# Kernel tuning notes

Measured on AMD Instinct MI355X. Metric: run time of the kernel, lower is better.

The kernel has to match this reference:

```python
import jax, jax.numpy as jnp
import numpy as np
from jax import lax

STRIDE = (1, 1)
PADDING = ((1, 1), (1, 1))
DILATION = (1, 1)


def setup_inputs() -> dict:
    key = jax.random.key(0)
    k1, k2 = jax.random.split(key)
    input = jax.random.normal(k1, (32, 128, 56, 56), dtype=jnp.float32)
    weight = jax.random.normal(k2, (256, 128, 3, 3), dtype=jnp.float32)
    bias = jnp.zeros((256,), dtype=jnp.float32)
    return {"input": input, "weight": weight, "bias": bias}


def reference(input, weight, bias):
    # The original builds the conv's dense matrix via conv2d on an identity
    # basis and then matmuls; that is mathematically identical to a direct
    # conv2d (the map is linear), plus the broadcast bias.
    out = lax.conv_general_dilated(
        input, weight,
        window_strides=STRIDE,
        padding=PADDING,
        rhs_dilation=DILATION,
        dimension_numbers=("NCHW", "OIHW", "NCHW"),
    )
    return out + bias[None, :, None, None]
```

## Files before the change

kernel.cpp:

```cpp
#include <hip/hip_runtime.h>
#include <hip/hip_bf16.h>
#include <stdint.h>


typedef __attribute__((ext_vector_type(8))) short bf16x8;
typedef __attribute__((ext_vector_type(8))) unsigned short ushort8;
typedef __attribute__((ext_vector_type(4))) float f32x4;

#define HW       56
#define SPATIAL  3136
#define C_IN     128
#define K_OUT    256
#define GEMM_K   1152
#define GEMM_N   100352

#define PHW      58
#define PIMG     3364
#define PADTOT_AL 107656

#define BM       256
#define BN       256
#define NTILE    18
#define BUFH     32768

__device__ __forceinline__ unsigned short f2bf(float f) {
    union { float f; unsigned int u; } v; v.f = f;
    unsigned int u = v.u + 0x7FFFu + ((v.u >> 16) & 1u);
    return (unsigned short)(u >> 16);
}

__device__ __forceinline__ void gload16(const unsigned short* g, unsigned short* l) {
    __builtin_amdgcn_global_load_lds(
        (const __attribute__((address_space(1))) unsigned int*)(g),
        (__attribute__((address_space(3))) unsigned int*)(l),
        16, 0, 0);
}

__global__ __launch_bounds__(256)
void prep_kernel(const float* __restrict__ w, unsigned short* __restrict__ w3,
                 unsigned short* __restrict__ pad) {
    if (blockIdx.x < 1152) {
        int idx = blockIdx.x * 256 + threadIdx.x;
        int rc   = idx / 18432;
        int rem  = idx % 18432;
        int tap  = rem / 2048;
        int rem2 = rem % 2048;
        int cc   = rem2 / 512;
        int s    = rem2 % 512;
        int l    = s >> 3, j = s & 7;
        int ko   = rc * 16 + (l & 15);
        int c    = cc * 32 + ((l >> 4) << 3) + j;
        w3[idx] = f2bf(w[(ko * C_IN + c) * 9 + tap]);
    } else {
        int idx = (blockIdx.x - 1152) * 256 + threadIdx.x;
        if (idx >= 29184) return;
        int cc  = idx / 7296;
        int r   = idx % 7296;
        int img = r / 228;
        int p   = r % 228;
        int pos;
        if (p < 58)       pos = p;
        else if (p < 116) pos = 57 * PHW + (p - 58);
        else { int i = p - 116; pos = (1 + (i >> 1)) * PHW + (i & 1) * 57; }
        unsigned short* d = pad + (size_t)cc * PADTOT_AL * 32
                          + ((size_t)img * PIMG + pos) * 32;
        const ushort8 z = (ushort8){0,0,0,0,0,0,0,0};
        *reinterpret_cast<ushort8*>(d)      = z;
        *reinterpret_cast<ushort8*>(d + 8)  = z;
        *reinterpret_cast<ushort8*>(d + 16) = z;
        *reinterpret_cast<ushort8*>(d + 24) = z;
    }
}

__global__ __launch_bounds__(256)
void intrans_kernel(const float* __restrict__ in, unsigned short* __restrict__ pad) {
    __shared__ __attribute__((aligned(16))) unsigned short l[56 * 136];
    const int bx = blockIdx.x;
    const int n = bx / HW, h = bx % HW;
    const int tid = threadIdx.x;
    const float* src = in + (size_t)n * C_IN * SPATIAL + h * HW;
    #pragma unroll
    for (int i = 0; i < 28; ++i) {
        int idx = i * 256 + tid;
        int c = idx / HW, w = idx % HW;
        l[w * 136 + c] = f2bf(src[(size_t)c * SPATIAL + w]);
    }
    __syncthreads();
    const int prow = n * PIMG + (h + 1) * PHW;
    #pragma unroll
    for (int j = 0; j < 4; ++j) {
        int chunk = j * 256 + tid;
        if (chunk < 896) {
            int w = chunk >> 4, c8 = chunk & 15;
            int cc = c8 >> 2, sub = c8 & 3;
            unsigned short* dst = pad + (size_t)cc * PADTOT_AL * 32
                                + (size_t)(prow + w + 1) * 32 + sub * 8;
            *reinterpret_cast<ushort8*>(dst) =
                *reinterpret_cast<const ushort8*>(&l[w * 136 + c8 * 8]);
        }
    }
}

__global__ __launch_bounds__(1024, 1)
void conv_tlp2(const unsigned short* __restrict__ pad,
               const unsigned short* __restrict__ w3,
               const float* __restrict__ bias,
               float* __restrict__ out) {
    __shared__ __attribute__((aligned(16))) unsigned short lds[2 * BUFH];

    const int tid  = threadIdx.x;
    const int wave = tid >> 6;
    const int lane = tid & 63;
    const int la   = lane & 15;
    const int lkh  = lane >> 4;

    const int bid = blockIdx.x;
    const int nt  = (bid & 7) * 49 + (bid >> 3);
    const int g0  = nt * BN;

    const int wr = wave >> 2, wc = wave & 3;

    const unsigned short* aw = w3 + (size_t)wave * 18432 + lane * 8;
    const unsigned short* bsrc;
    {
        int col = g0 + wave * 16 + la;
        int img = col / SPATIAL;
        int pos = col - img * SPATIAL;
        int oh  = pos / HW, ow = pos - oh * HW;
        bsrc = pad + (size_t)(img * PIMG + (oh + 1) * PHW + (ow + 1)) * 32 + lkh * 8;
    }

    f32x4 acc[4][4];
    #pragma unroll
    for (int i = 0; i < 4; ++i)
        #pragma unroll
        for (int j = 0; j < 4; ++j)
            acc[i][j] = (f32x4){0.f, 0.f, 0.f, 0.f};

    auto STAGE = [&](int tn, int kc) {
        const int tap = tn >> 1;
        const int cc  = (tn & 1) * 2 + kc;
        const int dr = tap / 3 - 1, dsx = tap % 3 - 1;
        unsigned short* dst = &lds[(tn & 1) * BUFH];
        gload16(aw + (size_t)(tap * 4 + cc) * 512, dst + (wave * 2 + kc) * 512);
        gload16(bsrc + (size_t)cc * (PADTOT_AL * 32) + (dr * PHW + dsx) * 32,
                dst + 16384 + (wave * 2 + kc) * 512);
    };

    bf16x8 af0[4], af1[4], bv0[4], bv1[4];

    STAGE(0, 0); STAGE(0, 1); STAGE(1, 0);
    asm volatile("s_waitcnt vmcnt(2)" ::: "memory");
    __builtin_amdgcn_s_barrier();

    #pragma unroll
    for (int t = 0; t < NTILE; ++t) {
        const unsigned short* Ab = &lds[(t & 1) * BUFH];

        #pragma unroll
        for (int mi = 0; mi < 4; ++mi)
            af0[mi] = *reinterpret_cast<const bf16x8*>(
                &Ab[((wr * 4 + mi) * 2 + 0) * 512 + lane * 8]);
        #pragma unroll
        for (int nj = 0; nj < 4; ++nj)
            bv0[nj] = *reinterpret_cast<const bf16x8*>(
                &Ab[16384 + ((wc * 4 + nj) * 2 + 0) * 512 + lane * 8]);
        #pragma unroll
        for (int mi = 0; mi < 4; ++mi)
            af1[mi] = *reinterpret_cast<const bf16x8*>(
                &Ab[((wr * 4 + mi) * 2 + 1) * 512 + lane * 8]);

        asm volatile("s_waitcnt lgkmcnt(4)" ::: "memory");
        __builtin_amdgcn_sched_barrier(0);
        __builtin_amdgcn_s_setprio(1);
        #pragma unroll
        for (int mi = 0; mi < 4; ++mi)
            #pragma unroll
            for (int nj = 0; nj < 4; ++nj)
                acc[mi][nj] = __builtin_amdgcn_mfma_f32_16x16x32_bf16(
                    af0[mi], bv0[nj], acc[mi][nj], 0, 0, 0);
        __builtin_amdgcn_s_setprio(0);

        __builtin_amdgcn_s_barrier();

        #pragma unroll
        for (int nj = 0; nj < 4; ++nj)
            bv1[nj] = *reinterpret_cast<const bf16x8*>(
                &Ab[16384 + ((wc * 4 + nj) * 2 + 1) * 512 + lane * 8]);
        if (t + 1 < NTILE) STAGE(t + 1, 1);
        if (t + 2 < NTILE) STAGE(t + 2, 0);

        asm volatile("s_waitcnt lgkmcnt(0)" ::: "memory");
        __builtin_amdgcn_sched_barrier(0);
        __builtin_amdgcn_s_setprio(1);
        #pragma unroll
        for (int mi = 0; mi < 4; ++mi)
            #pragma unroll
            for (int nj = 0; nj < 4; ++nj)
                acc[mi][nj] = __builtin_amdgcn_mfma_f32_16x16x32_bf16(
                    af1[mi], bv1[nj], acc[mi][nj], 0, 0, 0);
        __builtin_amdgcn_s_setprio(0);

        if (t < NTILE - 2) {
            asm volatile("s_waitcnt vmcnt(2)" ::: "memory");
            __builtin_amdgcn_s_barrier();
        } else if (t == NTILE - 2) {
            asm volatile("s_waitcnt vmcnt(0)" ::: "memory");
            __builtin_amdgcn_s_barrier();
        }
    }

    #pragma unroll
    for (int mi = 0; mi < 4; ++mi) {
        const int mb = wr * 64 + mi * 16 + lkh * 4;
        const f32x4 bv4 = *reinterpret_cast<const f32x4*>(&bias[mb]);
        #pragma unroll
        for (int nj = 0; nj < 4; ++nj) {
            const int gcol = g0 + wc * 64 + nj * 16;
            const int n2 = gcol / SPATIAL;
            const int p2 = gcol - n2 * SPATIAL + la;
            float* op = out + ((size_t)(n2 * K_OUT + mb)) * SPATIAL + p2;
            op[0]                   = acc[mi][nj][0] + bv4[0];
            op[SPATIAL]             = acc[mi][nj][1] + bv4[1];
            op[2 * SPATIAL]         = acc[mi][nj][2] + bv4[2];
            op[3 * (size_t)SPATIAL] = acc[mi][nj][3] + bv4[3];
        }
    }
}

#define LDK 40
__global__ __launch_bounds__(256)
void conv_mfma_fallback(const float* __restrict__ in,
                        const float* __restrict__ wraw,
                        const float* __restrict__ bias,
                        float* __restrict__ out) {
    __shared__ __attribute__((aligned(16))) unsigned short lA[128 * LDK];
    __shared__ __attribute__((aligned(16))) unsigned short lB[128 * LDK];
    const int tid = threadIdx.x;
    const int m0  = blockIdx.y * 128;
    const int g0  = blockIdx.x * 128;
    const int wave = tid >> 6, lane = tid & 63;
    const int wr = wave >> 1, wc = wave & 1;
    const int la = lane & 15, lkh = lane >> 4, lk = lkh * 8;

    f32x4 acc[4][4];
    #pragma unroll
    for (int i = 0; i < 4; ++i)
        #pragma unroll
        for (int j = 0; j < 4; ++j)
            acc[i][j] = (f32x4){0.f, 0.f, 0.f, 0.f};

    const int jj = tid & 127;
    const int kb = (tid >> 7) * 16;
    const int g = g0 + jj;
    const int nimg = g / SPATIAL;
    const int pos  = g % SPATIAL;
    const int oh = pos / HW, ow = pos % HW;

    for (int tap = 0; tap < 9; ++tap) {
        const int dr = tap / 3 - 1, dsx = tap % 3 - 1;
        const int ih = oh + dr, iw = ow + dsx;
        const bool valid = ((unsigned)ih < HW) && ((unsigned)iw < HW);
        const float* src = in + ((nimg * C_IN) * HW + ih) * HW + iw;
        for (int c0 = 0; c0 < C_IN; c0 += 32) {
            #pragma unroll
            for (int i = 0; i < 2; ++i) {
                const int ch = tid * 2 + i;
                const int row = ch >> 2;
                const int kp = (ch & 3) * 8;
                ushort8 v;
                #pragma unroll
                for (int e = 0; e < 8; ++e)
                    v[e] = f2bf(wraw[((m0 + row) * C_IN + c0 + kp + e) * 9 + tap]);
                *reinterpret_cast<ushort8*>(&lA[row * LDK + kp]) = v;
            }
            {
                ushort8 v0, v1;
                #pragma unroll
                for (int i = 0; i < 8; ++i)
                    v0[i] = f2bf(valid ? src[(c0 + kb + i) * SPATIAL] : 0.f);
                #pragma unroll
                for (int i = 0; i < 8; ++i)
                    v1[i] = f2bf(valid ? src[(c0 + kb + 8 + i) * SPATIAL] : 0.f);
                *reinterpret_cast<ushort8*>(&lB[jj * LDK + kb])     = v0;
                *reinterpret_cast<ushort8*>(&lB[jj * LDK + kb + 8]) = v1;
            }
            __syncthreads();
            bf16x8 af[4], bv[4];
            #pragma unroll
            for (int f = 0; f < 4; ++f) {
                af[f] = *reinterpret_cast<const bf16x8*>(&lA[(wr * 64 + f * 16 + la) * LDK + lk]);
                bv[f] = *reinterpret_cast<const bf16x8*>(&lB[(wc * 64 + f * 16 + la) * LDK + lk]);
            }
            #pragma unroll
            for (int fi = 0; fi < 4; ++fi)
                #pragma unroll
                for (int fj = 0; fj < 4; ++fj)
                    acc[fi][fj] = __builtin_amdgcn_mfma_f32_16x16x32_bf16(
                        af[fi], bv[fj], acc[fi][fj], 0, 0, 0);
            __syncthreads();
        }
    }
    const int mbase = m0 + wr * 64;
    const int cbase = g0 + wc * 64;
    #pragma unroll
    for (int fi = 0; fi < 4; ++fi) {
        float bvv[4];
        #pragma unroll
        for (int r = 0; r < 4; ++r)
            bvv[r] = bias[mbase + fi * 16 + lkh * 4 + r];
        #pragma unroll
        for (int fj = 0; fj < 4; ++fj) {
            const int gcol = cbase + fj * 16 + la;
            const int n2 = gcol / SPATIAL;
            const int p2 = gcol % SPATIAL;
            float* op = out + (size_t)(n2 * K_OUT) * SPATIAL + p2;
            #pragma unroll
            for (int r = 0; r < 4; ++r)
                op[(size_t)(mbase + fi * 16 + lkh * 4 + r) * SPATIAL] = acc[fi][fj][r] + bvv[r];
        }
    }
}

extern "C" void kernel_launch(void* const* d_in, const int* in_sizes, int n_in,
                              void* d_out, int out_size, void* d_ws, size_t ws_size,
                              hipStream_t stream) {
    const float* in   = (const float*)d_in[0];
    const float* w    = (const float*)d_in[1];
    const float* bias = (const float*)d_in[2];
    float* out = (float*)d_out;

    const size_t pad_halves = 4ull * PADTOT_AL * 32ull;
    const size_t need_bytes = (pad_halves + 294912ull) * 2ull;

    if (ws_size >= need_bytes) {
        unsigned short* pad = (unsigned short*)d_ws;
        unsigned short* w3  = pad + pad_halves;
        prep_kernel<<<1152 + 114, 256, 0, stream>>>(w, w3, pad);
        intrans_kernel<<<32 * HW, 256, 0, stream>>>(in, pad);
        conv_tlp2<<<GEMM_N / BN, 1024, 0, stream>>>(pad, w3, bias, out);
    } else {
        dim3 grid(GEMM_N / 128, K_OUT / 128);
        conv_mfma_fallback<<<grid, 256, 0, stream>>>(in, w, bias, out);
    }
}
```

Before: 98.86 us.

## Shrink conv GEMM tiles to 128x128 with two blocks per CU and merge prep kernels

Merges the weight-prep/pad-zero kernel and the input transpose kernel into one launch, removing a kernel boundary. Replaces the 1024-thread 256x256-tile conv kernel with a 512-thread 128x128-tile kernel split across M and N, with a swizzled block mapping and two blocks per CU. The goal is better occupancy, latency hiding and tail balance with a 1568-block grid. The cost is lower per-block data reuse and more global/LDS traffic per FLOP.

```diff
diff --git a/kernel.cpp b/kernel.cpp
--- a/kernel.cpp
+++ b/kernel.cpp
@@ -18,10 +18,10 @@
 #define PIMG     3364
 #define PADTOT_AL 107656
 
-#define BM       256
-#define BN       256
+#define BM       128
+#define BN       128
 #define NTILE    18
-#define BUFH     32768
+#define BUFH2    16384
 
 __device__ __forceinline__ unsigned short f2bf(float f) {
     union { float f; unsigned int u; } v; v.f = f;
@@ -37,22 +37,25 @@
 }
 
 __global__ __launch_bounds__(256)
-void prep_kernel(const float* __restrict__ w, unsigned short* __restrict__ w3,
-                 unsigned short* __restrict__ pad) {
-    if (blockIdx.x < 1152) {
-        int idx = blockIdx.x * 256 + threadIdx.x;
+void prep_all(const float* __restrict__ w, unsigned short* __restrict__ w3,
+              const float* __restrict__ in, unsigned short* __restrict__ pad) {
+    __shared__ __attribute__((aligned(16))) unsigned short l[56 * 136];
+    const int b = blockIdx.x;
+    const int tid = threadIdx.x;
+    if (b < 1152) {
+        int idx = b * 256 + tid;
         int rc   = idx / 18432;
         int rem  = idx % 18432;
         int tap  = rem / 2048;
         int rem2 = rem % 2048;
         int cc   = rem2 / 512;
         int s    = rem2 % 512;
-        int l    = s >> 3, j = s & 7;
-        int ko   = rc * 16 + (l & 15);
-        int c    = cc * 32 + ((l >> 4) << 3) + j;
+        int li   = s >> 3, j = s & 7;
+        int ko   = rc * 16 + (li & 15);
+        int c    = cc * 32 + ((li >> 4) << 3) + j;
         w3[idx] = f2bf(w[(ko * C_IN + c) * 9 + tap]);
-    } else {
-        int idx = (blockIdx.x - 1152) * 256 + threadIdx.x;
+    } else if (b < 1266) {
+        int idx = (b - 1152) * 256 + tid;
         if (idx >= 29184) return;
         int cc  = idx / 7296;
         int r   = idx % 7296;
@@ -69,44 +72,39 @@
         *reinterpret_cast<ushort8*>(d + 8)  = z;
         *reinterpret_cast<ushort8*>(d + 16) = z;
         *reinterpret_cast<ushort8*>(d + 24) = z;
-    }
-}
-
-__global__ __launch_bounds__(256)
-void intrans_kernel(const float* __restrict__ in, unsigned short* __restrict__ pad) {
-    __shared__ __attribute__((aligned(16))) unsigned short l[56 * 136];
-    const int bx = blockIdx.x;
-    const int n = bx / HW, h = bx % HW;
-    const int tid = threadIdx.x;
-    const float* src = in + (size_t)n * C_IN * SPATIAL + h * HW;
-    #pragma unroll
-    for (int i = 0; i < 28; ++i) {
-        int idx = i * 256 + tid;
-        int c = idx / HW, w = idx % HW;
-        l[w * 136 + c] = f2bf(src[(size_t)c * SPATIAL + w]);
-    }
-    __syncthreads();
-    const int prow = n * PIMG + (h + 1) * PHW;
-    #pragma unroll
-    for (int j = 0; j < 4; ++j) {
-        int chunk = j * 256 + tid;
-        if (chunk < 896) {
-            int w = chunk >> 4, c8 = chunk & 15;
-            int cc = c8 >> 2, sub = c8 & 3;
-            unsigned short* dst = pad + (size_t)cc * PADTOT_AL * 32
-                                + (size_t)(prow + w + 1) * 32 + sub * 8;
-            *reinterpret_cast<ushort8*>(dst) =
-                *reinterpret_cast<const ushort8*>(&l[w * 136 + c8 * 8]);
-        }
-    }
-}
-
-__global__ __launch_bounds__(1024, 1)
-void conv_tlp2(const unsigned short* __restrict__ pad,
-               const unsigned short* __restrict__ w3,
-               const float* __restrict__ bias,
-               float* __restrict__ out) {
-    __shared__ __attribute__((aligned(16))) unsigned short lds[2 * BUFH];
+    } else {
+        const int bx = b - 1266;
+        const int n = bx / HW, h = bx % HW;
+        const float* src = in + (size_t)n * C_IN * SPATIAL + h * HW;
+        #pragma unroll
+        for (int i = 0; i < 28; ++i) {
+            int idx = i * 256 + tid;
+            int c = idx / HW, wv = idx % HW;
+            l[wv * 136 + c] = f2bf(src[(size_t)c * SPATIAL + wv]);
+        }
+        __syncthreads();
+        const int prow = n * PIMG + (h + 1) * PHW;
+        #pragma unroll
+        for (int j = 0; j < 4; ++j) {
+            int chunk = j * 256 + tid;
+            if (chunk < 896) {
+                int wv = chunk >> 4, c8 = chunk & 15;
+                int cc = c8 >> 2, sub = c8 & 3;
+                unsigned short* dst = pad + (size_t)cc * PADTOT_AL * 32
+                                    + (size_t)(prow + wv + 1) * 32 + sub * 8;
+                *reinterpret_cast<ushort8*>(dst) =
+                    *reinterpret_cast<const ushort8*>(&l[wv * 136 + c8 * 8]);
+            }
+        }
+    }
+}
+
+__global__ __launch_bounds__(512, 2)
+void conv_2b(const unsigned short* __restrict__ pad,
+             const unsigned short* __restrict__ w3,
+             const float* __restrict__ bias,
+             float* __restrict__ out) {
+    __shared__ __attribute__((aligned(16))) unsigned short lds[2 * BUFH2];
 
     const int tid  = threadIdx.x;
     const int wave = tid >> 6;
@@ -115,12 +113,14 @@
     const int lkh  = lane >> 4;
 
     const int bid = blockIdx.x;
-    const int nt  = (bid & 7) * 49 + (bid >> 3);
+    const int swz = (bid & 7) * 196 + (bid >> 3);
+    const int mt  = swz & 1, nt = swz >> 1;
+    const int m0  = mt * BM;
     const int g0  = nt * BN;
 
     const int wr = wave >> 2, wc = wave & 3;
 
-    const unsigned short* aw = w3 + (size_t)wave * 18432 + lane * 8;
+    const unsigned short* aw = w3 + (size_t)(mt * 8 + wave) * 18432 + lane * 8;
     const unsigned short* bsrc;
     {
         int col = g0 + wave * 16 + la;
@@ -130,24 +130,24 @@
         bsrc = pad + (size_t)(img * PIMG + (oh + 1) * PHW + (ow + 1)) * 32 + lkh * 8;
     }
 
-    f32x4 acc[4][4];
+    f32x4 acc[4][2];
     #pragma unroll
     for (int i = 0; i < 4; ++i)
         #pragma unroll
-        for (int j = 0; j < 4; ++j)
+        for (int j = 0; j < 2; ++j)
             acc[i][j] = (f32x4){0.f, 0.f, 0.f, 0.f};
 
     auto STAGE = [&](int tn, int kc) {
         const int tap = tn >> 1;
         const int cc  = (tn & 1) * 2 + kc;
         const int dr = tap / 3 - 1, dsx = tap % 3 - 1;
-        unsigned short* dst = &lds[(tn & 1) * BUFH];
+        unsigned short* dst = &lds[(tn & 1) * BUFH2];
         gload16(aw + (size_t)(tap * 4 + cc) * 512, dst + (wave * 2 + kc) * 512);
         gload16(bsrc + (size_t)cc * (PADTOT_AL * 32) + (dr * PHW + dsx) * 32,
-                dst + 16384 + (wave * 2 + kc) * 512);
+                dst + 8192 + (wave * 2 + kc) * 512);
     };
 
-    bf16x8 af0[4], af1[4], bv0[4], bv1[4];
+    bf16x8 af0[4], af1[4], bv0[2], bv1[2];
 
     STAGE(0, 0); STAGE(0, 1); STAGE(1, 0);
     asm volatile("s_waitcnt vmcnt(2)" ::: "memory");
@@ -155,16 +155,16 @@
 
     #pragma unroll
     for (int t = 0; t < NTILE; ++t) {
-        const unsigned short* Ab = &lds[(t & 1) * BUFH];
+        const unsigned short* Ab = &lds[(t & 1) * BUFH2];
 
         #pragma unroll
         for (int mi = 0; mi < 4; ++mi)
             af0[mi] = *reinterpret_cast<const bf16x8*>(
                 &Ab[((wr * 4 + mi) * 2 + 0) * 512 + lane * 8]);
         #pragma unroll
-        for (int nj = 0; nj < 4; ++nj)
+        for (int nj = 0; nj < 2; ++nj)
             bv0[nj] = *reinterpret_cast<const bf16x8*>(
-                &Ab[16384 + ((wc * 4 + nj) * 2 + 0) * 512 + lane * 8]);
+                &Ab[8192 + ((wc * 2 + nj) * 2 + 0) * 512 + lane * 8]);
         #pragma unroll
         for (int mi = 0; mi < 4; ++mi)
             af1[mi] = *reinterpret_cast<const bf16x8*>(
@@ -176,7 +176,7 @@
         #pragma unroll
         for (int mi = 0; mi < 4; ++mi)
             #pragma unroll
-            for (int nj = 0; nj < 4; ++nj)
+            for (int nj = 0; nj < 2; ++nj)
                 acc[mi][nj] = __builtin_amdgcn_mfma_f32_16x16x32_bf16(
                     af0[mi], bv0[nj], acc[mi][nj], 0, 0, 0);
         __builtin_amdgcn_s_setprio(0);
@@ -184,9 +184,9 @@
         __builtin_amdgcn_s_barrier();
 
         #pragma unroll
-        for (int nj = 0; nj < 4; ++nj)
+        for (int nj = 0; nj < 2; ++nj)
             bv1[nj] = *reinterpret_cast<const bf16x8*>(
-                &Ab[16384 + ((wc * 4 + nj) * 2 + 1) * 512 + lane * 8]);
+                &Ab[8192 + ((wc * 2 + nj) * 2 + 1) * 512 + lane * 8]);
         if (t + 1 < NTILE) STAGE(t + 1, 1);
         if (t + 2 < NTILE) STAGE(t + 2, 0);
 
@@ -196,7 +196,7 @@
         #pragma unroll
         for (int mi = 0; mi < 4; ++mi)
             #pragma unroll
-            for (int nj = 0; nj < 4; ++nj)
+            for (int nj = 0; nj < 2; ++nj)
                 acc[mi][nj] = __builtin_amdgcn_mfma_f32_16x16x32_bf16(
                     af1[mi], bv1[nj], acc[mi][nj], 0, 0, 0);
         __builtin_amdgcn_s_setprio(0);
@@ -212,11 +212,11 @@
 
     #pragma unroll
     for (int mi = 0; mi < 4; ++mi) {
-        const int mb = wr * 64 + mi * 16 + lkh * 4;
+        const int mb = m0 + wr * 64 + mi * 16 + lkh * 4;
         const f32x4 bv4 = *reinterpret_cast<const f32x4*>(&bias[mb]);
         #pragma unroll
-        for (int nj = 0; nj < 4; ++nj) {
-            const int gcol = g0 + wc * 64 + nj * 16;
+        for (int nj = 0; nj < 2; ++nj) {
+            const int gcol = g0 + wc * 32 + nj * 16;
             const int n2 = gcol / SPATIAL;
             const int p2 = gcol - n2 * SPATIAL + la;
             float* op = out + ((size_t)(n2 * K_OUT + mb)) * SPATIAL + p2;
@@ -336,9 +336,8 @@
     if (ws_size >= need_bytes) {
         unsigned short* pad = (unsigned short*)d_ws;
         unsigned short* w3  = pad + pad_halves;
-        prep_kernel<<<1152 + 114, 256, 0, stream>>>(w, w3, pad);
-        intrans_kernel<<<32 * HW, 256, 0, stream>>>(in, pad);
-        conv_tlp2<<<GEMM_N / BN, 1024, 0, stream>>>(pad, w3, bias, out);
+        prep_all<<<1266 + 32 * HW, 256, 0, stream>>>(w, w3, in, pad);
+        conv_2b<<<(GEMM_N / BN) * (K_OUT / BM), 512, 0, stream>>>(pad, w3, bias, out);
     } else {
         dim3 grid(GEMM_N / 128, K_OUT / 128);
         conv_mfma_fallback<<<grid, 256, 0, stream>>>(in, w, bias, out);
```

Measured after the change: 98.21 us. About the same (-0.7%).
